# Kernel optimization log

Measured on AMD Instinct MI355X. Metric: run time of the kernel, lower is better.

## Reference

```python
import jax, jax.numpy as jnp
import numpy as np

NP_, NS_, DP_, DS_, DI_ = 16384, 8192, 256, 128, 128


def setup_inputs() -> dict:
    key = jax.random.key(0)
    ks = jax.random.split(key, 12)
    prot_node = jax.random.normal(ks[0], (NP_, DP_), dtype=jnp.float32)
    sub_node = jax.random.normal(ks[1], (NS_, DS_), dtype=jnp.float32)
    prot_idx = jax.random.randint(ks[2], (NP_,), 0, NP_, dtype=jnp.int32)
    sub_idx = jax.random.randint(ks[3], (NS_,), 0, NS_, dtype=jnp.int32)
    def lin(k, din, dout):
        return jax.random.normal(k, (din, dout), dtype=jnp.float32) / np.sqrt(din)
    return {
        "prot_node": prot_node,
        "sub_node": sub_node,
        "W_prot_proj": lin(ks[4], DP_, DI_),
        "b_prot_proj": jnp.zeros((DI_,), jnp.float32),
        "W_sub_proj": lin(ks[5], DS_, DI_),
        "b_sub_proj": jnp.zeros((DI_,), jnp.float32),
        "W_prot_out": lin(ks[6], DI_, DP_),
        "b_prot_out": jnp.zeros((DP_,), jnp.float32),
        "W_sub_out": lin(ks[7], DI_, DS_),
        "b_sub_out": jnp.zeros((DS_,), jnp.float32),
        "prot_idx": prot_idx,
        "sub_idx": sub_idx,
    }


def reference(prot_node, sub_node, W_prot_proj, b_prot_proj, W_sub_proj,
              b_sub_proj, W_prot_out, b_prot_out, W_sub_out, b_sub_out,
              prot_idx, sub_idx):
    # projections (dropout = identity at inference)
    prot_proj = prot_node @ W_prot_proj + b_prot_proj  # [Np, di]
    sub_proj = sub_node @ W_sub_proj + b_sub_proj      # [Ns, di]
    # additive score: sum_d(prot_int[i,d] + sub_int[j,d]) == rowsum_i + rowsum_j
    ps = jnp.sum(prot_proj[prot_idx], axis=-1)  # [Np]
    ss = jnp.sum(sub_proj[sub_idx], axis=-1)    # [Ns]
    scores = ps[:, None] + ss[None, :]          # [Np, Ns]
    prot_scores = jax.nn.softmax(scores, axis=1)        # [Np, Ns]
    sub_scores = jax.nn.softmax(scores, axis=0).T       # [Ns, Np]
    prot_out = (prot_scores @ sub_proj) @ W_prot_out + b_prot_out  # [Np, dp]
    sub_out = (sub_scores @ prot_proj) @ W_sub_out + b_sub_out     # [Ns, ds]
    return (prot_node + prot_out, prot_idx, sub_node + sub_out, sub_idx)
```

## Files before the change

### kernel.cpp

```cpp
#include <hip/hip_runtime.h>

#define NP 16384
#define NS 8192
#define DP 256
#define DS 128
#define DI 128

#define NBP 128
#define NBS 64

#define RP_OFF 0
#define RS_OFF (RP_OFF + NBP*DS)
#define ZP_OFF (RS_OFF + NBS*DP)
#define ZS_OFF (ZP_OFF + NBP)
#define BSC    (ZS_OFF + NBS)
#define BPC    (BSC + DS)

#define O1 (NP*DP)
#define O2 (O1 + NP)
#define O3 (O2 + NS*DS)
#define TOTAL (O3 + NS)
#define TOTAL4 (TOTAL/4)
#define GK2 1024
#define CHUNK (TOTAL4/GK2)

__device__ __forceinline__ float wsum64(float s) {
    #pragma unroll
    for (int m = 32; m >= 1; m >>= 1) s += __shfl_xor(s, m, 64);
    return s;
}

__global__ __launch_bounds__(512)
void k1(const float* __restrict__ pn, const float* __restrict__ sn,
        const float* __restrict__ Wpp, const float* __restrict__ bpp,
        const float* __restrict__ Wsp, const float* __restrict__ bsp,
        const float* __restrict__ Wpo, const float* __restrict__ bpo,
        const float* __restrict__ Wso, const float* __restrict__ bso,
        const int* __restrict__ pidx, const int* __restrict__ sidx,
        float* __restrict__ ws) {
    __shared__ float wcol[DP];
    __shared__ float racc[8 * DP];
    __shared__ float rz[8];
    __shared__ float acc2[DP];
    __shared__ float qv[DI];
    __shared__ float red[512];
    const int t = threadIdx.x;
    const int lane = t & 63;
    const int wv = t >> 6;
    const int b = blockIdx.x;

    if (b < NBP) {
        if (t < DP) {
            const float4* row = (const float4*)(Wpp + t * DI);
            float s = 0.f;
            #pragma unroll
            for (int d = 0; d < DI / 4; ++d) { float4 v = row[d]; s += v.x + v.y + v.z + v.w; }
            wcol[t] = s;
        }
        __syncthreads();
        const float4 wp = *(const float4*)(wcol + lane * 4);
        float4 acc = make_float4(0.f, 0.f, 0.f, 0.f);
        float z = 0.f;
        const int base = (b * 8 + wv) * 16;
        #pragma unroll
        for (int k = 0; k < 16; k += 2) {
            const int i0 = base + k, i1 = base + k + 1;
            const int g0 = pidx[i0], g1 = pidx[i1];
            const float4 x0 = *(const float4*)(pn + (size_t)g0 * DP + lane * 4);
            const float4 x1 = *(const float4*)(pn + (size_t)g1 * DP + lane * 4);
            float s0 = x0.x * wp.x + x0.y * wp.y + x0.z * wp.z + x0.w * wp.w;
            float s1 = x1.x * wp.x + x1.y * wp.y + x1.z * wp.z + x1.w * wp.w;
            #pragma unroll
            for (int m = 32; m >= 1; m >>= 1) {
                s0 += __shfl_xor(s0, m, 64);
                s1 += __shfl_xor(s1, m, 64);
            }
            const float e0 = __expf(s0), e1 = __expf(s1);
            const float4 y0 = *(const float4*)(pn + (size_t)i0 * DP + lane * 4);
            const float4 y1 = *(const float4*)(pn + (size_t)i1 * DP + lane * 4);
            acc.x += e0 * y0.x + e1 * y1.x;
            acc.y += e0 * y0.y + e1 * y1.y;
            acc.z += e0 * y0.z + e1 * y1.z;
            acc.w += e0 * y0.w + e1 * y1.w;
            z += e0 + e1;
        }
        ((float4*)(racc + wv * DP))[lane] = acc;
        if (lane == 0) rz[wv] = z;
        __syncthreads();
        if (t < DP) {
            float s = 0.f;
            #pragma unroll
            for (int w = 0; w < 8; ++w) s += racc[w * DP + t];
            acc2[t] = s;
        }
        if (t == 0) {
            float s = 0.f;
            #pragma unroll
            for (int w = 0; w < 8; ++w) s += rz[w];
            ws[ZP_OFF + b] = s;
        }
        __syncthreads();
        {
            const int d = t & 127, g = t >> 7;
            float a = 0.f;
            #pragma unroll 8
            for (int c = g * 64; c < g * 64 + 64; ++c) a += acc2[c] * Wpp[c * DI + d];
            red[t] = a;
        }
        __syncthreads();
        if (t < DI) qv[t] = red[t] + red[t + 128] + red[t + 256] + red[t + 384];
        __syncthreads();
        {
            const int c = t & 127, g = t >> 7;
            float a = 0.f;
            #pragma unroll 8
            for (int d = g * 32; d < g * 32 + 32; ++d) a += qv[d] * Wso[d * DS + c];
            red[t] = a;
        }
        __syncthreads();
        if (t < DS) ws[RP_OFF + b * DS + t] = red[t] + red[t + 128] + red[t + 256] + red[t + 384];
        if (b == 0) {
            __syncthreads();
            {
                const int c = t & 127, g = t >> 7;
                float a = 0.f;
                #pragma unroll 8
                for (int d = g * 32; d < g * 32 + 32; ++d) a += bpp[d] * Wso[d * DS + c];
                red[t] = a;
            }
            __syncthreads();
            if (t < DS) ws[BSC + t] = bso[t] + red[t] + red[t + 128] + red[t + 256] + red[t + 384];
        }
    } else {
        const int b2 = b - NBP;
        if (t < DS) {
            const float4* row = (const float4*)(Wsp + t * DI);
            float s = 0.f;
            #pragma unroll
            for (int d = 0; d < DI / 4; ++d) { float4 v = row[d]; s += v.x + v.y + v.z + v.w; }
            wcol[t] = s;
        }
        __syncthreads();
        const float2 wp = *(const float2*)(wcol + lane * 2);
        float2 acc = make_float2(0.f, 0.f);
        float z = 0.f;
        const int base = (b2 * 8 + wv) * 16;
        #pragma unroll
        for (int k = 0; k < 16; k += 2) {
            const int j0 = base + k, j1 = base + k + 1;
            const int g0 = sidx[j0], g1 = sidx[j1];
            const float2 x0 = *(const float2*)(sn + (size_t)g0 * DS + lane * 2);
            const float2 x1 = *(const float2*)(sn + (size_t)g1 * DS + lane * 2);
            float s0 = x0.x * wp.x + x0.y * wp.y;
            float s1 = x1.x * wp.x + x1.y * wp.y;
            #pragma unroll
            for (int m = 32; m >= 1; m >>= 1) {
                s0 += __shfl_xor(s0, m, 64);
                s1 += __shfl_xor(s1, m, 64);
            }
            const float e0 = __expf(s0), e1 = __expf(s1);
            const float2 y0 = *(const float2*)(sn + (size_t)j0 * DS + lane * 2);
            const float2 y1 = *(const float2*)(sn + (size_t)j1 * DS + lane * 2);
            acc.x += e0 * y0.x + e1 * y1.x;
            acc.y += e0 * y0.y + e1 * y1.y;
            z += e0 + e1;
        }
        ((float2*)(racc + wv * DS))[lane] = acc;
        if (lane == 0) rz[wv] = z;
        __syncthreads();
        if (t < DS) {
            float s = 0.f;
            #pragma unroll
            for (int w = 0; w < 8; ++w) s += racc[w * DS + t];
            acc2[t] = s;
        }
        if (t == 0) {
            float s = 0.f;
            #pragma unroll
            for (int w = 0; w < 8; ++w) s += rz[w];
            ws[ZS_OFF + b2] = s;
        }
        __syncthreads();
        {
            const int d = t & 127, g = t >> 7;
            float a = 0.f;
            #pragma unroll 8
            for (int c = g * 32; c < g * 32 + 32; ++c) a += acc2[c] * Wsp[c * DI + d];
            red[t] = a;
        }
        __syncthreads();
        if (t < DI) qv[t] = red[t] + red[t + 128] + red[t + 256] + red[t + 384];
        __syncthreads();
        {
            const int c = t & 255, g = t >> 8;
            float a = 0.f;
            #pragma unroll 8
            for (int d = g * 64; d < g * 64 + 64; ++d) a += qv[d] * Wpo[d * DP + c];
            red[t] = a;
        }
        __syncthreads();
        if (t < DP) ws[RS_OFF + b2 * DP + t] = red[t] + red[t + 256];
        if (b2 == 0) {
            __syncthreads();
            {
                const int c = t & 255, g = t >> 8;
                float a = 0.f;
                #pragma unroll 8
                for (int d = g * 64; d < g * 64 + 64; ++d) a += bsp[d] * Wpo[d * DP + c];
                red[t] = a;
            }
            __syncthreads();
            if (t < DP) ws[BPC + t] = bpo[t] + red[t] + red[t + 256];
        }
    }
}

__global__ __launch_bounds__(512)
void k2(const float* __restrict__ pn, const float* __restrict__ sn,
        const int* __restrict__ pidx, const int* __restrict__ sidx,
        const float* __restrict__ ws, float* __restrict__ out) {
    __shared__ float up[DP];
    __shared__ float us[DS];
    __shared__ float red[512];
    __shared__ float zsh[2];
    const int t = threadIdx.x;
    const int lane = t & 63;
    const int wv = t >> 6;
    const int b = blockIdx.x;
    const int start4 = b * CHUNK;
    const int end4 = start4 + CHUNK;

    if (wv == 0) {
        float z = ws[ZP_OFF + lane] + ws[ZP_OFF + 64 + lane];
        z = wsum64(z);
        if (lane == 0) zsh[0] = z;
    } else if (wv == 1) {
        float z = ws[ZS_OFF + lane];
        z = wsum64(z);
        if (lane == 0) zsh[1] = z;
    }
    __syncthreads();
    const float invZp = 1.f / zsh[0];
    const float invZs = 1.f / zsh[1];

    const bool needP = start4 < (O1 / 4);
    const bool needS = (end4 > (O2 / 4)) && (start4 < (O3 / 4));

    if (needP) {
        {
            const int c = t & 255, g = t >> 8;
            float a = 0.f;
            #pragma unroll 8
            for (int b2 = g * 32; b2 < g * 32 + 32; ++b2) a += ws[RS_OFF + b2 * DP + c];
            red[t] = a;
        }
        __syncthreads();
        if (t < DP) up[t] = ws[BPC + t] + invZs * (red[t] + red[t + 256]);
        __syncthreads();
    }
    if (needS) {
        {
            const int c = t & 127, g = t >> 7;
            float a = 0.f;
            #pragma unroll 8
            for (int b1 = g * 32; b1 < g * 32 + 32; ++b1) a += ws[RP_OFF + b1 * DS + c];
            red[t] = a;
        }
        __syncthreads();
        if (t < DS) us[t] = ws[BSC + t] + invZp * (red[t] + red[t + 128] + red[t + 256] + red[t + 384]);
        __syncthreads();
    }

    for (int g4 = start4 + t; g4 < end4; g4 += 512) {
        const int e4 = g4 * 4;
        float4 o;
        if (e4 < O1) {
            float4 x = *(const float4*)(pn + e4);
            int c = e4 & (DP - 1);
            o = make_float4(x.x + up[c], x.y + up[c + 1], x.z + up[c + 2], x.w + up[c + 3]);
        } else if (e4 < O2) {
            int i = e4 - O1;
            int4 v = *(const int4*)(pidx + i);
            o = make_float4((float)v.x, (float)v.y, (float)v.z, (float)v.w);
        } else if (e4 < O3) {
            int i = e4 - O2;
            float4 x = *(const float4*)(sn + i);
            int c = i & (DS - 1);
            o = make_float4(x.x + us[c], x.y + us[c + 1], x.z + us[c + 2], x.w + us[c + 3]);
        } else {
            int i = e4 - O3;
            int4 v = *(const int4*)(sidx + i);
            o = make_float4((float)v.x, (float)v.y, (float)v.z, (float)v.w);
        }
        *(float4*)(out + e4) = o;
    }
}

extern "C" void kernel_launch(void* const* d_in, const int* in_sizes, int n_in,
                              void* d_out, int out_size, void* d_ws, size_t ws_size,
                              hipStream_t stream) {
    const float* pn  = (const float*)d_in[0];
    const float* sn  = (const float*)d_in[1];
    const float* Wpp = (const float*)d_in[2];
    const float* bpp = (const float*)d_in[3];
    const float* Wsp = (const float*)d_in[4];
    const float* bsp = (const float*)d_in[5];
    const float* Wpo = (const float*)d_in[6];
    const float* bpo = (const float*)d_in[7];
    const float* Wso = (const float*)d_in[8];
    const float* bso = (const float*)d_in[9];
    const int* pidx  = (const int*)d_in[10];
    const int* sidx  = (const int*)d_in[11];
    float* ws  = (float*)d_ws;
    float* out = (float*)d_out;

    hipLaunchKernelGGL(k1, dim3(NBP + NBS), dim3(512), 0, stream,
                       pn, sn, Wpp, bpp, Wsp, bsp, Wpo, bpo, Wso, bso, pidx, sidx, ws);
    hipLaunchKernelGGL(k2, dim3(GK2), dim3(512), 0, stream,
                       pn, sn, pidx, sidx, ws, out);
}
```

Measured before the change: 30.33 us.

## Rebalance k1 grid to 256 blocks and prefetch k2 streaming loads before reductions

k1 now runs 256 blocks with a strided task loop, giving more blocks to the heavier protein side so the grid covers all CUs. k2 uses 512 blocks of 1024 threads, and each thread issues its three float4 loads before the shared-memory reductions of the partial results. This is meant to hide the latency of the streaming copy behind the reduction phase. The cost is more registers per thread and a larger reduction block, and the partial-sum loop counts (12 and 26) are hard-coded to the new block counts.

```diff
diff --git a/kernel.cpp b/kernel.cpp
--- a/kernel.cpp
+++ b/kernel.cpp
@@ -6,8 +6,13 @@
 #define DS 128
 #define DI 128
 
-#define NBP 128
-#define NBS 64
+#define NBP 208
+#define NBS 48
+#define G1  (NBP + NBS)
+#define NWP (NBP * 8)
+#define NWS (NBS * 8)
+#define TASKS_P (NP / 2)
+#define TASKS_S (NS / 2)
 
 #define RP_OFF 0
 #define RS_OFF (RP_OFF + NBP*DS)
@@ -21,14 +26,8 @@
 #define O3 (O2 + NS*DS)
 #define TOTAL (O3 + NS)
 #define TOTAL4 (TOTAL/4)
-#define GK2 1024
-#define CHUNK (TOTAL4/GK2)
-
-__device__ __forceinline__ float wsum64(float s) {
-    #pragma unroll
-    for (int m = 32; m >= 1; m >>= 1) s += __shfl_xor(s, m, 64);
-    return s;
-}
+#define G2  512
+#define CH4 (TOTAL4 / G2)
 
 __global__ __launch_bounds__(512)
 void k1(const float* __restrict__ pn, const float* __restrict__ sn,
@@ -61,10 +60,9 @@
         const float4 wp = *(const float4*)(wcol + lane * 4);
         float4 acc = make_float4(0.f, 0.f, 0.f, 0.f);
         float z = 0.f;
-        const int base = (b * 8 + wv) * 16;
-        #pragma unroll
-        for (int k = 0; k < 16; k += 2) {
-            const int i0 = base + k, i1 = base + k + 1;
+        const int wg = b * 8 + wv;
+        for (int tk = wg; tk < TASKS_P; tk += NWP) {
+            const int i0 = tk * 2, i1 = tk * 2 + 1;
             const int g0 = pidx[i0], g1 = pidx[i1];
             const float4 x0 = *(const float4*)(pn + (size_t)g0 * DP + lane * 4);
             const float4 x1 = *(const float4*)(pn + (size_t)g1 * DP + lane * 4);
@@ -144,10 +142,9 @@
         const float2 wp = *(const float2*)(wcol + lane * 2);
         float2 acc = make_float2(0.f, 0.f);
         float z = 0.f;
-        const int base = (b2 * 8 + wv) * 16;
-        #pragma unroll
-        for (int k = 0; k < 16; k += 2) {
-            const int j0 = base + k, j1 = base + k + 1;
+        const int wg = b2 * 8 + wv;
+        for (int tk = wg; tk < TASKS_S; tk += NWS) {
+            const int j0 = tk * 2, j1 = tk * 2 + 1;
             const int g0 = sidx[j0], g1 = sidx[j1];
             const float2 x0 = *(const float2*)(sn + (size_t)g0 * DS + lane * 2);
             const float2 x1 = *(const float2*)(sn + (size_t)g1 * DS + lane * 2);
@@ -215,28 +212,57 @@
     }
 }
 
-__global__ __launch_bounds__(512)
+__global__ __launch_bounds__(1024)
 void k2(const float* __restrict__ pn, const float* __restrict__ sn,
         const int* __restrict__ pidx, const int* __restrict__ sidx,
         const float* __restrict__ ws, float* __restrict__ out) {
     __shared__ float up[DP];
     __shared__ float us[DS];
-    __shared__ float red[512];
+    __shared__ float red[1024];
     __shared__ float zsh[2];
     const int t = threadIdx.x;
     const int lane = t & 63;
     const int wv = t >> 6;
     const int b = blockIdx.x;
-    const int start4 = b * CHUNK;
-    const int end4 = start4 + CHUNK;
+    const int start4 = b * CH4;
+    const int end4 = start4 + CH4;
+
+    float4 v0, v1, v2;
+    {
+        const int g0 = start4 + t, g1 = g0 + 1024, g2 = g1 + 1024;
+        {
+            const int e4 = g0 * 4;
+            v0 = (e4 < O1) ? *(const float4*)(pn + e4)
+               : (e4 < O2) ? *(const float4*)((const float*)pidx + (e4 - O1))
+               : (e4 < O3) ? *(const float4*)(sn + (e4 - O2))
+                           : *(const float4*)((const float*)sidx + (e4 - O3));
+        }
+        {
+            const int e4 = g1 * 4;
+            v1 = (e4 < O1) ? *(const float4*)(pn + e4)
+               : (e4 < O2) ? *(const float4*)((const float*)pidx + (e4 - O1))
+               : (e4 < O3) ? *(const float4*)(sn + (e4 - O2))
+                           : *(const float4*)((const float*)sidx + (e4 - O3));
+        }
+        if (g2 < end4) {
+            const int e4 = g2 * 4;
+            v2 = (e4 < O1) ? *(const float4*)(pn + e4)
+               : (e4 < O2) ? *(const float4*)((const float*)pidx + (e4 - O1))
+               : (e4 < O3) ? *(const float4*)(sn + (e4 - O2))
+                           : *(const float4*)((const float*)sidx + (e4 - O3));
+        }
+    }
 
     if (wv == 0) {
-        float z = ws[ZP_OFF + lane] + ws[ZP_OFF + 64 + lane];
-        z = wsum64(z);
+        float z = ws[ZP_OFF + lane] + ws[ZP_OFF + 64 + lane] + ws[ZP_OFF + 128 + lane]
+                + ((lane < NBP - 192) ? ws[ZP_OFF + 192 + lane] : 0.f);
+        #pragma unroll
+        for (int m = 32; m >= 1; m >>= 1) z += __shfl_xor(z, m, 64);
         if (lane == 0) zsh[0] = z;
     } else if (wv == 1) {
-        float z = ws[ZS_OFF + lane];
-        z = wsum64(z);
+        float z = (lane < NBS) ? ws[ZS_OFF + lane] : 0.f;
+        #pragma unroll
+        for (int m = 32; m >= 1; m >>= 1) z += __shfl_xor(z, m, 64);
         if (lane == 0) zsh[1] = z;
     }
     __syncthreads();
@@ -250,49 +276,57 @@
         {
             const int c = t & 255, g = t >> 8;
             float a = 0.f;
-            #pragma unroll 8
-            for (int b2 = g * 32; b2 < g * 32 + 32; ++b2) a += ws[RS_OFF + b2 * DP + c];
-            red[t] = a;
-        }
-        __syncthreads();
-        if (t < DP) up[t] = ws[BPC + t] + invZs * (red[t] + red[t + 256]);
+            #pragma unroll 4
+            for (int b2 = g * 12; b2 < g * 12 + 12; ++b2) a += ws[RS_OFF + b2 * DP + c];
+            red[t] = a;
+        }
+        __syncthreads();
+        if (t < DP) up[t] = ws[BPC + t] + invZs * (red[t] + red[t + 256] + red[t + 512] + red[t + 768]);
         __syncthreads();
     }
     if (needS) {
         {
             const int c = t & 127, g = t >> 7;
             float a = 0.f;
-            #pragma unroll 8
-            for (int b1 = g * 32; b1 < g * 32 + 32; ++b1) a += ws[RP_OFF + b1 * DS + c];
-            red[t] = a;
-        }
-        __syncthreads();
-        if (t < DS) us[t] = ws[BSC + t] + invZp * (red[t] + red[t + 128] + red[t + 256] + red[t + 384]);
-        __syncthreads();
-    }
-
-    for (int g4 = start4 + t; g4 < end4; g4 += 512) {
-        const int e4 = g4 * 4;
-        float4 o;
-        if (e4 < O1) {
-            float4 x = *(const float4*)(pn + e4);
-            int c = e4 & (DP - 1);
-            o = make_float4(x.x + up[c], x.y + up[c + 1], x.z + up[c + 2], x.w + up[c + 3]);
-        } else if (e4 < O2) {
-            int i = e4 - O1;
-            int4 v = *(const int4*)(pidx + i);
-            o = make_float4((float)v.x, (float)v.y, (float)v.z, (float)v.w);
-        } else if (e4 < O3) {
-            int i = e4 - O2;
-            float4 x = *(const float4*)(sn + i);
-            int c = i & (DS - 1);
-            o = make_float4(x.x + us[c], x.y + us[c + 1], x.z + us[c + 2], x.w + us[c + 3]);
-        } else {
-            int i = e4 - O3;
-            int4 v = *(const int4*)(sidx + i);
-            o = make_float4((float)v.x, (float)v.y, (float)v.z, (float)v.w);
-        }
-        *(float4*)(out + e4) = o;
+            #pragma unroll 4
+            for (int b1 = g * 26; b1 < g * 26 + 26; ++b1) a += ws[RP_OFF + b1 * DS + c];
+            red[t] = a;
+        }
+        __syncthreads();
+        if (t < DS) {
+            float s = 0.f;
+            #pragma unroll
+            for (int g = 0; g < 8; ++g) s += red[t + 128 * g];
+            us[t] = ws[BSC + t] + invZp * s;
+        }
+    }
+    __syncthreads();
+
+    {
+        const int g4s[3] = { start4 + t, start4 + t + 1024, start4 + t + 2048 };
+        const float4 vs[3] = { v0, v1, v2 };
+        #pragma unroll
+        for (int k = 0; k < 3; ++k) {
+            const int g4 = g4s[k];
+            if (k == 2 && g4 >= end4) break;
+            const int e4 = g4 * 4;
+            const float4 x = vs[k];
+            float4 o;
+            if (e4 < O1) {
+                const int c = e4 & (DP - 1);
+                o = make_float4(x.x + up[c], x.y + up[c + 1], x.z + up[c + 2], x.w + up[c + 3]);
+            } else if (e4 < O2) {
+                o = make_float4((float)__float_as_int(x.x), (float)__float_as_int(x.y),
+                                (float)__float_as_int(x.z), (float)__float_as_int(x.w));
+            } else if (e4 < O3) {
+                const int c = (e4 - O2) & (DS - 1);
+                o = make_float4(x.x + us[c], x.y + us[c + 1], x.z + us[c + 2], x.w + us[c + 3]);
+            } else {
+                o = make_float4((float)__float_as_int(x.x), (float)__float_as_int(x.y),
+                                (float)__float_as_int(x.z), (float)__float_as_int(x.w));
+            }
+            *(float4*)(out + e4) = o;
+        }
     }
 }
 
@@ -314,8 +348,8 @@
     float* ws  = (float*)d_ws;
     float* out = (float*)d_out;
 
-    hipLaunchKernelGGL(k1, dim3(NBP + NBS), dim3(512), 0, stream,
+    hipLaunchKernelGGL(k1, dim3(G1), dim3(512), 0, stream,
                        pn, sn, Wpp, bpp, Wsp, bsp, Wpo, bpo, Wso, bso, pidx, sidx, ws);
-    hipLaunchKernelGGL(k2, dim3(GK2), dim3(512), 0, stream,
+    hipLaunchKernelGGL(k2, dim3(G2), dim3(1024), 0, stream,
                        pn, sn, pidx, sidx, ws, out);
 }
```

Result: slower. 36.78 us (+21.3%).
